# Performance work log

Hardware: AMD Instinct MI355X
Metric: run time of the kernel (lower is better)

Reference implementation:

```python
import jax, jax.numpy as jnp
import numpy as np

D_MODEL = 1024
N_STATE = 1024


def setup_inputs() -> dict:
    key = jax.random.key(0)
    k_x, k_A, k_Bw, k_Bb, k_Cw, k_Cb = jax.random.split(key, 6)
    x = jax.random.normal(k_x, (8, 2048, D_MODEL), dtype=jnp.float32)
    log_A = jax.random.normal(k_A, (N_STATE,), dtype=jnp.float32) * 0.1 - 1.0
    # nn.Linear default init: U(-1/sqrt(fan_in), 1/sqrt(fan_in)); weight is [out, in]
    bnd_B = 1.0 / np.sqrt(D_MODEL)
    B_w = jax.random.uniform(k_Bw, (N_STATE, D_MODEL), minval=-bnd_B, maxval=bnd_B, dtype=jnp.float32)
    B_b = jax.random.uniform(k_Bb, (N_STATE,), minval=-bnd_B, maxval=bnd_B, dtype=jnp.float32)
    bnd_C = 1.0 / np.sqrt(N_STATE)
    C_w = jax.random.uniform(k_Cw, (D_MODEL, N_STATE), minval=-bnd_C, maxval=bnd_C, dtype=jnp.float32)
    C_b = jax.random.uniform(k_Cb, (D_MODEL,), minval=-bnd_C, maxval=bnd_C, dtype=jnp.float32)
    return {"x": x, "log_A": log_A, "B_w": B_w, "B_b": B_b, "C_w": C_w, "C_b": C_b}


def _ssm_scan(A, B_x):
    """Diagonal linear recurrence h_t = A * h_{t-1} + B_x_t (h_0 prior = 0).

    Implemented as a parallel associative scan over the time axis.
    A: [N], B_x: [B, T, N] -> h: [B, T, N]
    """
    a = jnp.broadcast_to(A, B_x.shape)  # [B, T, N]

    def combine(c1, c2):
        a1, b1 = c1
        a2, b2 = c2
        return (a1 * a2, a2 * b1 + b2)

    _, h = jax.lax.associative_scan(combine, (a, B_x), axis=1)
    return h


def reference(x, log_A, B_w, B_b, C_w, C_b):
    A = jax.nn.sigmoid(log_A)                                  # [N]
    B_x = jnp.einsum('btd,nd->btn', x, B_w) + B_b              # [B, T, N]
    h = _ssm_scan(A, B_x)                                      # [B, T, N]
    y = jnp.einsum('btn,dn->btd', h, C_w) + C_b                # [B, T, D]
    return y
```

## Files before the change

kernel.cpp:

```cpp
#include <hip/hip_runtime.h>
#include <hip/hip_bf16.h>
#include <cstdint>
#include <cstddef>


typedef __attribute__((ext_vector_type(8))) short short8;
typedef __attribute__((ext_vector_type(4))) float f32x4;

#define AS_GLOBAL(p) ((const __attribute__((address_space(1))) void*)(p))
#define AS_LDS(p)    ((__attribute__((address_space(3))) void*)(p))

__device__ __forceinline__ unsigned short f2bf(float f) {
    union { float f; unsigned u; } v; v.f = f;
    return (unsigned short)((v.u + 0x7FFFu + ((v.u >> 16) & 1u)) >> 16);
}
__device__ __forceinline__ float bf2f(unsigned short u) {
    union { float f; unsigned u; } v; v.u = ((unsigned)u) << 16;
    return v.f;
}

__global__ void cvt_all(const float4* __restrict__ x, const float4* __restrict__ bw,
                        const float4* __restrict__ cw, ushort4* __restrict__ xo,
                        ushort4* __restrict__ bo, ushort4* __restrict__ co) {
    const int NX = (16384 * 1024) / 4;
    const int NW = (1024 * 1024) / 4;
    int i = blockIdx.x * blockDim.x + threadIdx.x;
    int stride = gridDim.x * blockDim.x;
    for (; i < NX + 2 * NW; i += stride) {
        const float4* s; ushort4* d; int j;
        if (i < NX)           { s = x;  d = xo; j = i; }
        else if (i < NX + NW) { s = bw; d = bo; j = i - NX; }
        else                  { s = cw; d = co; j = i - NX - NW; }
        float4 v = s[j];
        d[j] = make_ushort4(f2bf(v.x), f2bf(v.y), f2bf(v.z), f2bf(v.w));
    }
}

__global__ __launch_bounds__(256, 2)
void gemm1_scan_fused(const unsigned short* __restrict__ A,
                      const unsigned short* __restrict__ B,
                      const float* __restrict__ bias,
                      const float* __restrict__ logA,
                      unsigned short* __restrict__ H,
                      int M, int N, int K)
{
    constexpr int BK = 32, SXS = 130;
    __shared__ __align__(16) unsigned short smem[20800];
    unsigned short* As = smem;
    unsigned short* Bs = smem + 5120;
    unsigned short* Sx = smem;

    const int tid  = threadIdx.x;
    const int lane = tid & 63;
    const int wave = tid >> 6;
    const int wr   = wave >> 1;
    const int wm   = wr * 64;
    const int wn   = (wave & 1) * 64;
    const int q    = lane >> 4;
    const int l16  = lane & 15;
    const int m0   = blockIdx.x * 128;
    const int n0   = blockIdx.y * 128;

    const int rsub = lane >> 2;
    const int c8   = (lane & 3) * 8;

    f32x4 acc[4][4] = {};
    f32x4 accw[4]   = {};

    for (int k0 = 0; k0 < K; k0 += BK) {
        #pragma unroll
        for (int p = 0; p < 2; ++p) {
            const int rowbase = p * 64 + wave * 16;
            int gra = m0 - 32 + rowbase + rsub; if (gra < 0) gra = 0;
            const unsigned short* ga = A + (size_t)gra * K + k0 + c8;
            const unsigned short* gb = B + (size_t)(n0 + rowbase + rsub) * K + k0 + c8;
            __builtin_amdgcn_global_load_lds(AS_GLOBAL(ga), AS_LDS(&As[rowbase * BK]), 16, 0, 0);
            __builtin_amdgcn_global_load_lds(AS_GLOBAL(gb), AS_LDS(&Bs[rowbase * BK]), 16, 0, 0);
        }
        if (tid < 128) {
            const int rowbase = 128 + wave * 16;
            const unsigned short* ga = A + (size_t)(m0 - 32 + rowbase + rsub) * K + k0 + c8;
            __builtin_amdgcn_global_load_lds(AS_GLOBAL(ga), AS_LDS(&As[rowbase * BK]), 16, 0, 0);
        }
        __syncthreads();

        short8 a[4], aw, b[4];
        #pragma unroll
        for (int i = 0; i < 4; ++i)
            a[i] = *reinterpret_cast<const short8*>(&As[(32 + wm + i * 16 + l16) * BK + q * 8]);
        aw = *reinterpret_cast<const short8*>(&As[(wr * 16 + l16) * BK + q * 8]);
        #pragma unroll
        for (int j = 0; j < 4; ++j)
            b[j] = *reinterpret_cast<const short8*>(&Bs[(wn + j * 16 + l16) * BK + q * 8]);

        #pragma unroll
        for (int i = 0; i < 4; ++i)
            #pragma unroll
            for (int j = 0; j < 4; ++j)
                acc[i][j] = __builtin_amdgcn_mfma_f32_16x16x32_bf16(a[i], b[j], acc[i][j], 0, 0, 0);
        #pragma unroll
        for (int j = 0; j < 4; ++j)
            accw[j] = __builtin_amdgcn_mfma_f32_16x16x32_bf16(aw, b[j], accw[j], 0, 0, 0);
        __syncthreads();
    }

    float bcol[4];
    #pragma unroll
    for (int j = 0; j < 4; ++j)
        bcol[j] = bias[n0 + wn + j * 16 + l16];

    #pragma unroll
    for (int j = 0; j < 4; ++j) {
        #pragma unroll
        for (int r = 0; r < 4; ++r)
            Sx[(wr * 16 + q * 4 + r) * SXS + wn + j * 16 + l16] = f2bf(accw[j][r] + bcol[j]);
        #pragma unroll
        for (int i = 0; i < 4; ++i)
            #pragma unroll
            for (int r = 0; r < 4; ++r)
                Sx[(32 + wm + i * 16 + q * 4 + r) * SXS + wn + j * 16 + l16] = f2bf(acc[i][j][r] + bcol[j]);
    }
    __syncthreads();

    const int col  = tid & 127;
    const int half = tid >> 7;
    const int n    = n0 + col;
    const float Aa = 1.0f / (1.0f + __expf(-logA[n]));
    const bool chunk0 = (blockIdx.x & 15) == 0;

    float h = 0.0f;
    const int rw = half ? 64 : 0;
    if (!(half == 0 && chunk0)) {
        #pragma unroll
        for (int r = 0; r < 32; ++r)
            h = fmaf(Aa, h, bf2f(Sx[(rw + r) * SXS + col]));
    }
    const int rs = half ? 96 : 32;
    size_t o = (size_t)(m0 + (half ? 64 : 0)) * 1024 + n;
    #pragma unroll 8
    for (int r = 0; r < 64; ++r) {
        h = fmaf(Aa, h, bf2f(Sx[(rs + r) * SXS + col]));
        H[o] = f2bf(h);
        o += 1024;
    }
}

__global__ __launch_bounds__(512, 2)
void gemm2_8ph(const unsigned short* __restrict__ A,
               const unsigned short* __restrict__ B,
               const float* __restrict__ bias,
               float* __restrict__ C,
               int M, int N, int K)
{
    constexpr int BK  = 64;
    constexpr int NKT = 16;
    __shared__ __align__(16) unsigned short As[4 * 8192];
    __shared__ __align__(16) unsigned short Bs[4 * 8192];

    const int tid  = threadIdx.x;
    const int lane = tid & 63;
    const int wave = tid >> 6;
    const int wg   = wave >> 2;
    const int wm   = wg * 128;
    const int wn   = (wave & 3) * 64;
    const int hB   = wn >> 7;
    const int bR0  = wn & 127;
    const int q    = lane >> 4;
    const int l16  = lane & 15;
    const int swx  = (l16 & 7) << 4;
    const int m0   = blockIdx.x * 256;
    const int n0   = blockIdx.y * 256;

    const unsigned short* aSrc[2];
    const unsigned short* bSrc[2];
    int dDst[2];
    #pragma unroll
    for (int p = 0; p < 2; ++p) {
        const int d = tid * 16 + p * 8192;
        const int l = d ^ (((d >> 7) & 7) << 4);
        const int srow = l >> 7;
        const int scol = (l & 127) >> 1;
        aSrc[p] = A + (size_t)(m0 + srow) * K + scol;
        bSrc[p] = B + (size_t)(n0 + srow) * K + scol;
        dDst[p] = d;
    }

    char* ldsA = (char*)As;
    char* ldsB = (char*)Bs;

    auto stageA = [&](int h, int kt) {
        const int slot = ((2 * kt + h) & 3) << 14;
        #pragma unroll
        for (int p = 0; p < 2; ++p)
            __builtin_amdgcn_global_load_lds(
                AS_GLOBAL(aSrc[p] + (size_t)h * 128 * K + kt * 64),
                AS_LDS(ldsA + slot + dDst[p]), 16, 0, 0);
    };
    auto stageB = [&](int h, int kt) {
        const int slot = ((2 * kt + h) & 3) << 14;
        #pragma unroll
        for (int p = 0; p < 2; ++p)
            __builtin_amdgcn_global_load_lds(
                AS_GLOBAL(bSrc[p] + (size_t)h * 128 * K + kt * 64),
                AS_LDS(ldsB + slot + dDst[p]), 16, 0, 0);
    };

    f32x4 acc[8][4] = {};

    stageA(0, 0); stageA(1, 0); stageB(0, 0); stageB(1, 0);
    stageA(0, 1); stageA(1, 1); stageB(0, 1); stageB(1, 1);
    asm volatile("s_waitcnt vmcnt(8)" ::: "memory");
    __builtin_amdgcn_s_barrier();

    #pragma unroll 1
    for (int kt = 0; kt < NKT; ++kt) {
        const int aSlot = ((2 * kt + wg) & 3) << 14;
        const int bSlot = ((2 * kt + hB) & 3) << 14;
        short8 bfrag[4][2];
        #pragma unroll
        for (int p = 0; p < 4; ++p) {
            short8 afrag[2][2];
            #pragma unroll
            for (int i2 = 0; i2 < 2; ++i2)
                #pragma unroll
                for (int ks = 0; ks < 2; ++ks) {
                    const int row = (p * 2 + i2) * 16 + l16;
                    const int lby = row * 128 + ks * 64 + q * 16;
                    afrag[i2][ks] = *reinterpret_cast<const short8*>(ldsA + aSlot + (lby ^ swx));
                }
            if (p == 0) {
                #pragma unroll
                for (int j = 0; j < 4; ++j)
                    #pragma unroll
                    for (int ks = 0; ks < 2; ++ks) {
                        const int row = bR0 + j * 16 + l16;
                        const int lby = row * 128 + ks * 64 + q * 16;
                        bfrag[j][ks] = *reinterpret_cast<const short8*>(ldsB + bSlot + (lby ^ swx));
                    }
            }
            if (p == 0) { if (kt >= 1 && kt + 1 < NKT) stageA(0, kt + 1); }
            if (p == 1) { if (kt >= 1 && kt + 1 < NKT) stageA(1, kt + 1); }
            if (p == 2) { if (kt + 2 < NKT) stageB(0, kt + 2); }
            if (p == 3) {
                if (kt + 2 < NKT) stageB(1, kt + 2);
                if (kt < NKT - 2)       asm volatile("s_waitcnt vmcnt(4)" ::: "memory");
                else if (kt == NKT - 2) asm volatile("s_waitcnt vmcnt(0)" ::: "memory");
            }
            __builtin_amdgcn_s_barrier();
            asm volatile("s_waitcnt lgkmcnt(0)" ::: "memory");
            __builtin_amdgcn_s_setprio(1);
            #pragma unroll
            for (int ks = 0; ks < 2; ++ks)
                #pragma unroll
                for (int i2 = 0; i2 < 2; ++i2)
                    #pragma unroll
                    for (int j = 0; j < 4; ++j)
                        acc[p * 2 + i2][j] = __builtin_amdgcn_mfma_f32_16x16x32_bf16(
                            afrag[i2][ks], bfrag[j][ks], acc[p * 2 + i2][j], 0, 0, 0);
            __builtin_amdgcn_s_setprio(0);
            __builtin_amdgcn_s_barrier();
        }
    }

    float bcol[4];
    #pragma unroll
    for (int j = 0; j < 4; ++j)
        bcol[j] = bias[n0 + wn + j * 16 + l16];

    #pragma unroll
    for (int i = 0; i < 8; ++i) {
        const int r0 = m0 + wm + i * 16 + q * 4;
        #pragma unroll
        for (int j = 0; j < 4; ++j) {
            const int col = n0 + wn + j * 16 + l16;
            #pragma unroll
            for (int r = 0; r < 4; ++r)
                C[(size_t)(r0 + r) * N + col] = acc[i][j][r] + bcol[j];
        }
    }
}

__global__ __launch_bounds__(256)
void ssm_scan(const float* __restrict__ Bx,
              const float* __restrict__ logA,
              unsigned short* __restrict__ H)
{
    constexpr int T = 2048, NS = 1024, L = 64, W = 32;
    const int tid   = threadIdx.x;
    const int bi    = blockIdx.x;
    const int ng    = bi & 3;
    const int chunk = (bi >> 2) & 31;
    const int b     = bi >> 7;
    const int n     = ng * 256 + tid;

    const float Aa = 1.0f / (1.0f + __expf(-logA[n]));
    const int t0 = chunk * L;
    int tw = t0 - W; if (tw < 0) tw = 0;

    const size_t base = (size_t)b * T * NS + n;
    float h = 0.0f;
    for (int t = tw; t < t0; ++t)
        h = fmaf(Aa, h, Bx[base + (size_t)t * NS]);

    const float* src = Bx + base + (size_t)t0 * NS;
    unsigned short* dst = H + base + (size_t)t0 * NS;
    #pragma unroll 8
    for (int t = 0; t < L; ++t) {
        h = fmaf(Aa, h, src[(size_t)t * NS]);
        dst[(size_t)t * NS] = f2bf(h);
    }
}

extern "C" void kernel_launch(void* const* d_in, const int* in_sizes, int n_in,
                              void* d_out, int out_size, void* d_ws, size_t ws_size,
                              hipStream_t stream)
{
    const float* x    = (const float*)d_in[0];
    const float* logA = (const float*)d_in[1];
    const float* Bw   = (const float*)d_in[2];
    const float* Bb   = (const float*)d_in[3];
    const float* Cw   = (const float*)d_in[4];
    const float* Cb   = (const float*)d_in[5];
    float* out = (float*)d_out;

    const int M = 8 * 2048, N = 1024, K = 1024;

    unsigned short* xh  = (unsigned short*)d_ws;
    unsigned short* Bwb = xh + (size_t)M * K;
    unsigned short* Cwb = Bwb + (size_t)N * K;
    unsigned short* hb  = Cwb + (size_t)N * K;

    const size_t need_fused = ((size_t)M * K * 2 + (size_t)N * K * 2) * 2 + (size_t)N * K * 2;

    cvt_all<<<4096, 256, 0, stream>>>((const float4*)x, (const float4*)Bw,
                                      (const float4*)Cw, (ushort4*)xh,
                                      (ushort4*)Bwb, (ushort4*)Cwb);

    dim3 grid1(M / 128, N / 128);
    dim3 grid2(M / 256, N / 256);
    if (ws_size >= need_fused) {
        gemm1_scan_fused<<<grid1, 256, 0, stream>>>(xh, Bwb, Bb, logA, hb, M, N, K);
        gemm2_8ph<<<grid2, 512, 0, stream>>>(hb, Cwb, Cb, out, M, N, K);
    } else {
        gemm2_8ph<<<grid2, 512, 0, stream>>>(xh, Bwb, Bb, out, M, N, K);
        ssm_scan<<<1024, 256, 0, stream>>>(out, logA, xh);
        gemm2_8ph<<<grid2, 512, 0, stream>>>(xh, Cwb, Cb, out, M, N, K);
    }
}
```

Baseline: 226.3 us.

## Port fused GEMM1+scan onto 256x256 multi-stage pipelined LDS schedule

Replaces the simple 128x128 single-buffered GEMM1 with the same 8-phase, 4-slot, swizzled-LDS pipelined structure used by GEMM2. Tiles grow to 256x256 with 512 threads, and a 32-row warmup halo is staged separately. The scan epilogue now covers 256 columns and 128-row halves. This is meant to hide global-load latency and raise MFMA utilisation. In exchange it uses about 146KB of LDS, which limits occupancy, and adds more complex waitcnt and barrier logic.

After: 202.8 us. 10.4% less time.

```diff
diff --git a/kernel.cpp b/kernel.cpp
--- a/kernel.cpp
+++ b/kernel.cpp
@@ -36,72 +36,145 @@
     }
 }
 
-__global__ __launch_bounds__(256, 2)
-void gemm1_scan_fused(const unsigned short* __restrict__ A,
-                      const unsigned short* __restrict__ B,
-                      const float* __restrict__ bias,
-                      const float* __restrict__ logA,
-                      unsigned short* __restrict__ H,
-                      int M, int N, int K)
+__global__ __launch_bounds__(512, 2)
+void gemm1_8ph_scan(const unsigned short* __restrict__ A,
+                    const unsigned short* __restrict__ B,
+                    const float* __restrict__ bias,
+                    const float* __restrict__ logA,
+                    unsigned short* __restrict__ H,
+                    int M, int N, int K)
 {
-    constexpr int BK = 32, SXS = 130;
-    __shared__ __align__(16) unsigned short smem[20800];
-    unsigned short* As = smem;
-    unsigned short* Bs = smem + 5120;
-    unsigned short* Sx = smem;
+    constexpr int NKT = 16;
+    constexpr int SXS = 260;
+    __shared__ __align__(16) char smem[149760];
+    char* ldsA = smem;
+    char* ldsB = smem + 65536;
+    char* ldsW = smem + 131072;
+    unsigned short* Sx = (unsigned short*)smem;
 
     const int tid  = threadIdx.x;
     const int lane = tid & 63;
     const int wave = tid >> 6;
-    const int wr   = wave >> 1;
-    const int wm   = wr * 64;
-    const int wn   = (wave & 1) * 64;
+    const int wg   = wave >> 2;
+    const int wm   = wg * 128;
+    const int wn   = (wave & 3) * 64;
+    const int hB   = wn >> 7;
+    const int bR0  = wn & 127;
     const int q    = lane >> 4;
     const int l16  = lane & 15;
-    const int m0   = blockIdx.x * 128;
-    const int n0   = blockIdx.y * 128;
-
-    const int rsub = lane >> 2;
-    const int c8   = (lane & 3) * 8;
-
-    f32x4 acc[4][4] = {};
+    const int swx  = (l16 & 7) << 4;
+    const int m0   = blockIdx.x * 256;
+    const int n0   = blockIdx.y * 256;
+
+    const unsigned short* aSrc[2];
+    const unsigned short* bSrc[2];
+    int dDst[2];
+    #pragma unroll
+    for (int p = 0; p < 2; ++p) {
+        const int d = tid * 16 + p * 8192;
+        const int l = d ^ (((d >> 7) & 7) << 4);
+        const int srow = l >> 7;
+        const int scol = (l & 127) >> 1;
+        aSrc[p] = A + (size_t)(m0 + srow) * K + scol;
+        bSrc[p] = B + (size_t)(n0 + srow) * K + scol;
+        dDst[p] = d;
+    }
+    const int dW = wave * 512 + lane * 16;
+    const int lW = dW ^ (((dW >> 7) & 7) << 4);
+    int wrow = m0 - 32 + (lW >> 7); if (wrow < 0) wrow = 0;
+    const unsigned short* wSrc = A + (size_t)wrow * K + ((lW & 127) >> 1);
+
+    auto stageA = [&](int h, int kt) {
+        const int slot = ((2 * kt + h) & 3) << 14;
+        #pragma unroll
+        for (int p = 0; p < 2; ++p)
+            __builtin_amdgcn_global_load_lds(
+                AS_GLOBAL(aSrc[p] + (size_t)h * 128 * K + kt * 64),
+                AS_LDS(ldsA + slot + dDst[p]), 16, 0, 0);
+    };
+    auto stageB = [&](int h, int kt) {
+        const int slot = ((2 * kt + h) & 3) << 14;
+        #pragma unroll
+        for (int p = 0; p < 2; ++p)
+            __builtin_amdgcn_global_load_lds(
+                AS_GLOBAL(bSrc[p] + (size_t)h * 128 * K + kt * 64),
+                AS_LDS(ldsB + slot + dDst[p]), 16, 0, 0);
+    };
+    auto stageW = [&](int kt) {
+        if (lane < 32)
+            __builtin_amdgcn_global_load_lds(
+                AS_GLOBAL(wSrc + kt * 64),
+                AS_LDS(ldsW + ((kt & 1) << 12) + dW), 16, 0, 0);
+    };
+
+    f32x4 acc[8][4] = {};
     f32x4 accw[4]   = {};
 
-    for (int k0 = 0; k0 < K; k0 += BK) {
-        #pragma unroll
-        for (int p = 0; p < 2; ++p) {
-            const int rowbase = p * 64 + wave * 16;
-            int gra = m0 - 32 + rowbase + rsub; if (gra < 0) gra = 0;
-            const unsigned short* ga = A + (size_t)gra * K + k0 + c8;
-            const unsigned short* gb = B + (size_t)(n0 + rowbase + rsub) * K + k0 + c8;
-            __builtin_amdgcn_global_load_lds(AS_GLOBAL(ga), AS_LDS(&As[rowbase * BK]), 16, 0, 0);
-            __builtin_amdgcn_global_load_lds(AS_GLOBAL(gb), AS_LDS(&Bs[rowbase * BK]), 16, 0, 0);
+    stageA(0, 0); stageA(1, 0); stageW(0); stageB(0, 0); stageB(1, 0);
+    stageA(0, 1); stageA(1, 1); stageW(1); stageB(0, 1); stageB(1, 1);
+    asm volatile("s_waitcnt vmcnt(9)" ::: "memory");
+    __builtin_amdgcn_s_barrier();
+
+    #pragma unroll 1
+    for (int kt = 0; kt < NKT; ++kt) {
+        const int aSlot = ((2 * kt + wg) & 3) << 14;
+        const int bSlot = ((2 * kt + hB) & 3) << 14;
+        const int wSlot = (kt & 1) << 12;
+        short8 bfrag[4][2];
+        short8 aw[2];
+        #pragma unroll
+        for (int p = 0; p < 4; ++p) {
+            short8 afrag[2][2];
+            #pragma unroll
+            for (int i2 = 0; i2 < 2; ++i2)
+                #pragma unroll
+                for (int ks = 0; ks < 2; ++ks) {
+                    const int row = (p * 2 + i2) * 16 + l16;
+                    const int lby = row * 128 + ks * 64 + q * 16;
+                    afrag[i2][ks] = *reinterpret_cast<const short8*>(ldsA + aSlot + (lby ^ swx));
+                }
+            if (p == 0) {
+                #pragma unroll
+                for (int j = 0; j < 4; ++j)
+                    #pragma unroll
+                    for (int ks = 0; ks < 2; ++ks) {
+                        const int row = bR0 + j * 16 + l16;
+                        const int lby = row * 128 + ks * 64 + q * 16;
+                        bfrag[j][ks] = *reinterpret_cast<const short8*>(ldsB + bSlot + (lby ^ swx));
+                    }
+                #pragma unroll
+                for (int ks = 0; ks < 2; ++ks) {
+                    const int row = wg * 16 + l16;
+                    const int lby = row * 128 + ks * 64 + q * 16;
+                    aw[ks] = *reinterpret_cast<const short8*>(ldsW + wSlot + (lby ^ swx));
+                }
+            }
+            if (p == 0 && kt >= 1 && kt + 1 < NKT) { stageA(0, kt + 1); stageW(kt + 1); }
+            if (p == 1 && kt >= 1 && kt + 1 < NKT) stageA(1, kt + 1);
+            if (p == 2 && kt + 2 < NKT) stageB(0, kt + 2);
+            if (p == 3) {
+                if (kt + 2 < NKT) stageB(1, kt + 2);
+                if (kt < NKT - 2)       asm volatile("s_waitcnt vmcnt(4)" ::: "memory");
+                else if (kt == NKT - 2) asm volatile("s_waitcnt vmcnt(0)" ::: "memory");
+            }
+            __builtin_amdgcn_s_barrier();
+            asm volatile("s_waitcnt lgkmcnt(0)" ::: "memory");
+            __builtin_amdgcn_s_setprio(1);
+            #pragma unroll
+            for (int ks = 0; ks < 2; ++ks)
+                #pragma unroll
+                for (int i2 = 0; i2 < 2; ++i2)
+                    #pragma unroll
+                    for (int j = 0; j < 4; ++j)
+                        acc[p * 2 + i2][j] = __builtin_amdgcn_mfma_f32_16x16x32_bf16(
+                            afrag[i2][ks], bfrag[j][ks], acc[p * 2 + i2][j], 0, 0, 0);
+            #pragma unroll
+            for (int ks = 0; ks < 2; ++ks)
+                accw[p] = __builtin_amdgcn_mfma_f32_16x16x32_bf16(
+                    aw[ks], bfrag[p][ks], accw[p], 0, 0, 0);
+            __builtin_amdgcn_s_setprio(0);
+            __builtin_amdgcn_s_barrier();
         }
-        if (tid < 128) {
-            const int rowbase = 128 + wave * 16;
-            const unsigned short* ga = A + (size_t)(m0 - 32 + rowbase + rsub) * K + k0 + c8;
-            __builtin_amdgcn_global_load_lds(AS_GLOBAL(ga), AS_LDS(&As[rowbase * BK]), 16, 0, 0);
-        }
-        __syncthreads();
-
-        short8 a[4], aw, b[4];
-        #pragma unroll
-        for (int i = 0; i < 4; ++i)
-            a[i] = *reinterpret_cast<const short8*>(&As[(32 + wm + i * 16 + l16) * BK + q * 8]);
-        aw = *reinterpret_cast<const short8*>(&As[(wr * 16 + l16) * BK + q * 8]);
-        #pragma unroll
-        for (int j = 0; j < 4; ++j)
-            b[j] = *reinterpret_cast<const short8*>(&Bs[(wn + j * 16 + l16) * BK + q * 8]);
-
-        #pragma unroll
-        for (int i = 0; i < 4; ++i)
-            #pragma unroll
-            for (int j = 0; j < 4; ++j)
-                acc[i][j] = __builtin_amdgcn_mfma_f32_16x16x32_bf16(a[i], b[j], acc[i][j], 0, 0, 0);
-        #pragma unroll
-        for (int j = 0; j < 4; ++j)
-            accw[j] = __builtin_amdgcn_mfma_f32_16x16x32_bf16(aw, b[j], accw[j], 0, 0, 0);
-        __syncthreads();
     }
 
     float bcol[4];
@@ -113,32 +186,32 @@
     for (int j = 0; j < 4; ++j) {
         #pragma unroll
         for (int r = 0; r < 4; ++r)
-            Sx[(wr * 16 + q * 4 + r) * SXS + wn + j * 16 + l16] = f2bf(accw[j][r] + bcol[j]);
-        #pragma unroll
-        for (int i = 0; i < 4; ++i)
+            Sx[(wg * 16 + q * 4 + r) * SXS + wn + j * 16 + l16] = f2bf(accw[j][r] + bcol[j]);
+        #pragma unroll
+        for (int i = 0; i < 8; ++i)
             #pragma unroll
             for (int r = 0; r < 4; ++r)
                 Sx[(32 + wm + i * 16 + q * 4 + r) * SXS + wn + j * 16 + l16] = f2bf(acc[i][j][r] + bcol[j]);
     }
     __syncthreads();
 
-    const int col  = tid & 127;
-    const int half = tid >> 7;
+    const int col  = tid & 255;
+    const int half = tid >> 8;
     const int n    = n0 + col;
     const float Aa = 1.0f / (1.0f + __expf(-logA[n]));
-    const bool chunk0 = (blockIdx.x & 15) == 0;
+    const bool chunk0 = (blockIdx.x & 7) == 0;
 
     float h = 0.0f;
-    const int rw = half ? 64 : 0;
+    const int rw = half ? 128 : 0;
     if (!(half == 0 && chunk0)) {
         #pragma unroll
         for (int r = 0; r < 32; ++r)
             h = fmaf(Aa, h, bf2f(Sx[(rw + r) * SXS + col]));
     }
-    const int rs = half ? 96 : 32;
-    size_t o = (size_t)(m0 + (half ? 64 : 0)) * 1024 + n;
+    const int rs = half ? 160 : 32;
+    size_t o = (size_t)(m0 + (half ? 128 : 0)) * 1024 + n;
     #pragma unroll 8
-    for (int r = 0; r < 64; ++r) {
+    for (int r = 0; r < 128; ++r) {
         h = fmaf(Aa, h, bf2f(Sx[(rs + r) * SXS + col]));
         H[o] = f2bf(h);
         o += 1024;
@@ -152,7 +225,6 @@
                float* __restrict__ C,
                int M, int N, int K)
 {
-    constexpr int BK  = 64;
     constexpr int NKT = 16;
     __shared__ __align__(16) unsigned short As[4 * 8192];
     __shared__ __align__(16) unsigned short Bs[4 * 8192];
@@ -336,10 +408,10 @@
                                       (const float4*)Cw, (ushort4*)xh,
                                       (ushort4*)Bwb, (ushort4*)Cwb);
 
-    dim3 grid1(M / 128, N / 128);
+    dim3 grid1(M / 256, N / 256);
     dim3 grid2(M / 256, N / 256);
     if (ws_size >= need_fused) {
-        gemm1_scan_fused<<<grid1, 256, 0, stream>>>(xh, Bwb, Bb, logA, hb, M, N, K);
+        gemm1_8ph_scan<<<grid1, 512, 0, stream>>>(xh, Bwb, Bb, logA, hb, M, N, K);
         gemm2_8ph<<<grid2, 512, 0, stream>>>(hb, Cwb, Cb, out, M, N, K);
     } else {
         gemm2_8ph<<<grid2, 512, 0, stream>>>(xh, Bwb, Bb, out, M, N, K);
```
